# Kernel optimization log

Hardware: AMD Instinct MI355X
Metric: run time of the kernel (lower is better)

Reference implementation:

```python
import jax, jax.numpy as jnp
import numpy as np
from jax import lax

T, B, D, H = 1024, 64, 512, 1024


def setup_inputs() -> dict:
    key = jax.random.key(0)
    ks = jax.random.split(key, 5)
    x = jax.random.normal(ks[0], (T, B, D), dtype=jnp.float32)
    W_ih_0 = jax.random.normal(ks[1], (H, D), dtype=jnp.float32) * (1.0 / np.sqrt(D))
    w_hh_0 = jax.random.uniform(ks[2], (H,), dtype=jnp.float32)
    b_0 = jnp.zeros((H,), dtype=jnp.float32)
    W_ih_1 = jax.random.normal(ks[3], (H, H), dtype=jnp.float32) * (1.0 / np.sqrt(H))
    w_hh_1 = jax.random.uniform(ks[4], (H,), dtype=jnp.float32)
    b_1 = jnp.zeros((H,), dtype=jnp.float32)
    return {"x": x, "W_ih_0": W_ih_0, "w_hh_0": w_hh_0, "b_0": b_0,
            "W_ih_1": W_ih_1, "w_hh_1": w_hh_1, "b_1": b_1}


def _indrnn_layer(x, W_ih, w_hh, b):
    # Hoist the input projection into one batched GEMM over all timesteps.
    pre = jnp.einsum('tbd,hd->tbh', x, W_ih) + b  # [T,B,H]
    h0 = jnp.zeros((x.shape[1], W_ih.shape[0]), dtype=x.dtype)

    def step(h, p):
        h_new = jnp.tanh(p + h * w_hh)  # diagonal recurrence
        return h_new, h_new

    _, out = lax.scan(step, h0, pre)  # out: [T,B,H]
    return out


def reference(x, W_ih_0, w_hh_0, b_0, W_ih_1, w_hh_1, b_1):
    out0 = _indrnn_layer(x, W_ih_0, w_hh_0, b_0)
    out1 = _indrnn_layer(out0, W_ih_1, w_hh_1, b_1)
    # Original returns (last-layer outputs, initial hidden) -- hidden is
    # the unchanged zeros tensor of shape [num_layers, B, H].
    hidden = jnp.zeros((2, x.shape[1], W_ih_0.shape[0]), dtype=x.dtype)
    return out1, hidden
```

## Files before the change

### kernel.cpp

```cpp
#include <hip/hip_runtime.h>
#include <hip/hip_fp16.h>
#include <cstdint>
#include <cstddef>

#define TT 1024
#define BB 64
#define DD 512
#define HH 1024
#define MM (TT * BB)

typedef _Float16 f16;
typedef _Float16 f16x8 __attribute__((ext_vector_type(8)));
typedef float f32x4 __attribute__((ext_vector_type(4)));

__global__ void cvt_f32_to_f16(const float* __restrict__ src,
                               f16* __restrict__ dst, int n) {
    int i = blockIdx.x * blockDim.x + threadIdx.x;
    int idx = i * 8;
    if (idx + 8 <= n) {
        float4 a = *reinterpret_cast<const float4*>(src + idx);
        float4 b = *reinterpret_cast<const float4*>(src + idx + 4);
        f16x8 o;
        o[0] = (f16)a.x; o[1] = (f16)a.y; o[2] = (f16)a.z; o[3] = (f16)a.w;
        o[4] = (f16)b.x; o[5] = (f16)b.y; o[6] = (f16)b.z; o[7] = (f16)b.w;
        *reinterpret_cast<f16x8*>(dst + idx) = o;
    } else {
        for (int k = idx; k < n; ++k) dst[k] = (f16)src[k];
    }
}

__global__ void cvt_weights(const float* __restrict__ W0, f16* __restrict__ W0h,
                            int n0, const float* __restrict__ W1,
                            f16* __restrict__ W1h) {
    int i = blockIdx.x * blockDim.x + threadIdx.x;
    int idx = i * 8;
    const float* s;
    f16* d;
    int off;
    if (idx < n0) { s = W0; d = W0h; off = idx; }
    else          { s = W1; d = W1h; off = idx - n0; }
    float4 a = *reinterpret_cast<const float4*>(s + off);
    float4 b = *reinterpret_cast<const float4*>(s + off + 4);
    f16x8 o;
    o[0] = (f16)a.x; o[1] = (f16)a.y; o[2] = (f16)a.z; o[3] = (f16)a.w;
    o[4] = (f16)b.x; o[5] = (f16)b.y; o[6] = (f16)b.z; o[7] = (f16)b.w;
    *reinterpret_cast<f16x8*>(d + off) = o;
}

__device__ __forceinline__ void gload16(const void* g, void* l) {
    __builtin_amdgcn_global_load_lds(
        (const __attribute__((address_space(1))) void*)g,
        (__attribute__((address_space(3))) void*)l, 16, 0, 0);
}

__device__ __forceinline__ void stage128x64(const f16* __restrict__ G,
                                            int rowbase, int K, int kt,
                                            f16* lbuf, int tid) {
    #pragma unroll
    for (int j = 0; j < 4; ++j) {
        int p   = (j * 256 + tid) * 16;
        int row = p >> 7;
        int lc  = (p & 127) ^ ((row & 7) << 4);
        gload16(G + (size_t)(rowbase + row) * K + kt * 64 + (lc >> 1),
                (char*)lbuf + p);
    }
}

__device__ __forceinline__ f16x8 ldfrag(const f16* buf, int r, int s,
                                        int kg) {
    int c = ((s * 4 + kg) ^ (r & 7)) << 4;
    return *reinterpret_cast<const f16x8*>((const char*)buf + r * 128 + c);
}

template <typename TC>
__global__ __launch_bounds__(256, 4) void gemm5(
    const f16* __restrict__ A, const f16* __restrict__ W,
    const float* __restrict__ bias, TC* __restrict__ C,
    int M, int N, int K) {
    __shared__ f16 lds[2][128 * 64];

    const int tid  = threadIdx.x;
    const int lane = tid & 63;
    const int wid  = tid >> 6;
    const int wm   = wid >> 1;
    const int wn   = wid & 1;
    const int lr   = lane & 15;
    const int kg   = lane >> 4;

    const int nwg = gridDim.x;
    int bid = blockIdx.x;
    int wg  = (nwg % 8 == 0) ? ((bid & 7) * (nwg >> 3) + (bid >> 3)) : bid;
    const int ncol = N >> 7;
    const int brow = (wg / ncol) << 7;
    const int bcol = (wg % ncol) << 7;

    const int NT = K >> 6;

    f32x4 acc[4][4] = {};

    for (int t = 0; t < NT; ++t) {
        __syncthreads();
        stage128x64(A, brow, K, t, lds[0], tid);
        stage128x64(W, bcol, K, t, lds[1], tid);
        __syncthreads();

        #pragma unroll
        for (int s = 0; s < 2; ++s) {
            f16x8 af[4], bf[4];
            #pragma unroll
            for (int m = 0; m < 4; ++m)
                af[m] = ldfrag(lds[0], wm * 64 + m * 16 + lr, s, kg);
            #pragma unroll
            for (int n = 0; n < 4; ++n)
                bf[n] = ldfrag(lds[1], wn * 64 + n * 16 + lr, s, kg);
            #pragma unroll
            for (int m = 0; m < 4; ++m)
                #pragma unroll
                for (int n = 0; n < 4; ++n)
                    acc[m][n] = __builtin_amdgcn_mfma_f32_16x16x32_f16(
                        af[m], bf[n], acc[m][n], 0, 0, 0);
        }
    }

    if constexpr (sizeof(TC) == 2) {
        f16* Ct = &lds[0][0];
        __syncthreads();
        #pragma unroll
        for (int fn = 0; fn < 4; ++fn) {
            int col = wn * 64 + fn * 16 + lr;
            float bv = bias[bcol + col];
            #pragma unroll
            for (int fm = 0; fm < 4; ++fm) {
                int row0 = wm * 64 + fm * 16 + kg * 4;
                #pragma unroll
                for (int j = 0; j < 4; ++j) {
                    int r  = row0 + j;
                    int pb = r * 256 + ((col * 2) ^ ((r & 7) << 4));
                    *(f16*)((char*)Ct + pb) = (f16)(acc[fm][fn][j] + bv);
                }
            }
        }
        __syncthreads();
        #pragma unroll
        for (int i = 0; i < 8; ++i) {
            int e   = (i * 256 + tid) * 16;
            int row = e >> 8;
            int cb  = e & 255;
            int pb  = row * 256 + (cb ^ ((row & 7) << 4));
            f16x8 v = *(const f16x8*)((const char*)Ct + pb);
            *reinterpret_cast<f16x8*>(
                (f16*)C + (size_t)(brow + row) * N + bcol + (cb >> 1)) = v;
        }
    } else {
        #pragma unroll
        for (int fn = 0; fn < 4; ++fn) {
            int col = bcol + wn * 64 + fn * 16 + lr;
            float bv = bias[col];
            #pragma unroll
            for (int fm = 0; fm < 4; ++fm) {
                int row0 = brow + wm * 64 + fm * 16 + kg * 4;
                #pragma unroll
                for (int j = 0; j < 4; ++j)
                    C[(size_t)(row0 + j) * N + col] = (TC)(acc[fm][fn][j] + bv);
            }
        }
    }
}

__device__ __forceinline__ float fast_tanh(float x) {
    float e = __builtin_amdgcn_exp2f(x * 2.8853900817779268f);
    float r = __builtin_amdgcn_rcpf(e + 1.0f);
    return 1.0f - 2.0f * r;
}

template <typename TI, typename TO, int PF, bool ZTAIL>
__global__ __launch_bounds__(256) void scan_kernel(
    const TI* __restrict__ pre, const float* __restrict__ w,
    TO* __restrict__ out) {
    const int S = BB * HH;
    const int idx = blockIdx.x * blockDim.x + threadIdx.x;
    const float wv = w[idx & (HH - 1)];
    const TI* p = pre + idx;
    TO* o = out + idx;

    float buf[PF];
    #pragma unroll
    for (int i = 0; i < PF; ++i) buf[i] = (float)p[(size_t)i * S];

    float h = 0.f;
    for (int t0 = 0; t0 < TT; t0 += PF) {
        float nbuf[PF];
        #pragma unroll
        for (int i = 0; i < PF; ++i) {
            int tp = t0 + PF + i;
            tp = (tp < TT - 1) ? tp : (TT - 1);
            nbuf[i] = (float)p[(size_t)tp * S];
        }
        #pragma unroll
        for (int i = 0; i < PF; ++i) {
            h = fast_tanh(fmaf(h, wv, buf[i]));
            o[(size_t)(t0 + i) * S] = (TO)h;
        }
        #pragma unroll
        for (int i = 0; i < PF; ++i) buf[i] = nbuf[i];
    }
    if constexpr (ZTAIL) {
        o[(size_t)TT * S] = (TO)0.f;
        o[(size_t)(TT + 1) * S] = (TO)0.f;
    }
}

extern "C" void kernel_launch(void* const* d_in, const int* in_sizes, int n_in,
                              void* d_out, int out_size, void* d_ws, size_t ws_size,
                              hipStream_t stream) {
    const float* x  = (const float*)d_in[0];
    const float* W0 = (const float*)d_in[1];
    const float* w0 = (const float*)d_in[2];
    const float* b0 = (const float*)d_in[3];
    const float* W1 = (const float*)d_in[4];
    const float* w1 = (const float*)d_in[5];
    const float* b1 = (const float*)d_in[6];
    float* out = (float*)d_out;

    const size_t SZ_big = (size_t)MM * HH * sizeof(f16);
    const size_t O_W0   = SZ_big;
    const size_t O_W1   = O_W0 + (size_t)HH * DD * sizeof(f16);
    const size_t O_pre1 = O_W1 + (size_t)HH * HH * sizeof(f16);
    const bool f16pre1  = (ws_size >= O_pre1 + SZ_big);

    f16* big   = (f16*)d_ws;
    f16* W0h   = (f16*)((char*)d_ws + O_W0);
    f16* W1h   = (f16*)((char*)d_ws + O_W1);
    f16* pre1h = (f16*)((char*)d_ws + O_pre1);

    const int nwg = (MM / 128) * (HH / 128);

    cvt_f32_to_f16<<<(MM * DD) / 8 / 256, 256, 0, stream>>>(x, big, MM * DD);
    cvt_weights<<<(HH * DD + HH * HH) / 8 / 256, 256, 0, stream>>>(
        W0, W0h, HH * DD, W1, W1h);

    gemm5<f16><<<nwg, 256, 0, stream>>>(big, W0h, b0, (f16*)d_out, MM, HH, DD);

    scan_kernel<f16, f16, 32, false><<<(BB * HH) / 256, 256, 0, stream>>>(
        (const f16*)d_out, w0, big);

    if (f16pre1) {
        gemm5<f16><<<nwg, 256, 0, stream>>>(big, W1h, b1, pre1h, MM, HH, HH);
        scan_kernel<f16, float, 32, true><<<(BB * HH) / 256, 256, 0, stream>>>(
            pre1h, w1, out);
    } else {
        gemm5<float><<<nwg, 256, 0, stream>>>(big, W1h, b1, out, MM, HH, HH);
        scan_kernel<float, float, 32, true><<<(BB * HH) / 256, 256, 0, stream>>>(
            out, w1, out);
    }
}
```

Measured before the change: 425.4 us.

## Add 128x256-tile triple-buffered GEMM with split MFMA phases for layer-1 projection

Adds a new gemm8 kernel for the second layer's input projection (K=1024). It uses 512 threads, 128x256 output tiles and a three-stage LDS ring buffer, and staggers the A and B global-to-LDS loads between two MFMA half-phases. It also raises wave priority during the MFMA bursts. The aim is to increase per-tile data reuse and hide global load latency better than the 128x128 double-buffered gemm5. In exchange it uses 144KB of LDS, which allows only one workgroup per CU and halves the grid size. Only the f16 pre1 path uses it; the fp32 fallback still uses gemm5.

```diff
diff --git a/kernel.cpp b/kernel.cpp
--- a/kernel.cpp
+++ b/kernel.cpp
@@ -53,6 +53,12 @@
         (__attribute__((address_space(3))) void*)l, 16, 0, 0);
 }
 
+__device__ __forceinline__ f16x8 ldfrag(const f16* buf, int r, int s,
+                                        int kg) {
+    int c = ((s * 4 + kg) ^ (r & 7)) << 4;
+    return *reinterpret_cast<const f16x8*>((const char*)buf + r * 128 + c);
+}
+
 __device__ __forceinline__ void stage128x64(const f16* __restrict__ G,
                                             int rowbase, int K, int kt,
                                             f16* lbuf, int tid) {
@@ -64,12 +70,6 @@
         gload16(G + (size_t)(rowbase + row) * K + kt * 64 + (lc >> 1),
                 (char*)lbuf + p);
     }
-}
-
-__device__ __forceinline__ f16x8 ldfrag(const f16* buf, int r, int s,
-                                        int kg) {
-    int c = ((s * 4 + kg) ^ (r & 7)) << 4;
-    return *reinterpret_cast<const f16x8*>((const char*)buf + r * 128 + c);
 }
 
 template <typename TC>
@@ -164,6 +164,154 @@
                     C[(size_t)(row0 + j) * N + col] = (TC)(acc[fm][fn][j] + bv);
             }
         }
+    }
+}
+
+__device__ __forceinline__ void stageA8(const f16* __restrict__ G,
+                                        int rowbase, int K, int kt,
+                                        f16* lbuf, int tid) {
+    #pragma unroll
+    for (int j = 0; j < 2; ++j) {
+        int p   = (j * 512 + tid) * 16;
+        int row = p >> 7;
+        int lc  = (p & 127) ^ ((row & 7) << 4);
+        gload16(G + (size_t)(rowbase + row) * K + kt * 64 + (lc >> 1),
+                (char*)lbuf + p);
+    }
+}
+__device__ __forceinline__ void stageB8(const f16* __restrict__ G,
+                                        int rowbase, int K, int kt,
+                                        f16* lbuf, int tid) {
+    #pragma unroll
+    for (int j = 0; j < 4; ++j) {
+        int p   = (j * 512 + tid) * 16;
+        int row = p >> 7;
+        int lc  = (p & 127) ^ ((row & 7) << 4);
+        gload16(G + (size_t)(rowbase + row) * K + kt * 64 + (lc >> 1),
+                (char*)lbuf + p);
+    }
+}
+
+__global__ __launch_bounds__(512, 1) void gemm8(
+    const f16* __restrict__ A, const f16* __restrict__ W,
+    const float* __restrict__ bias, f16* __restrict__ C,
+    int M, int N, int K) {
+    __shared__ __align__(16) char smem[3 * 49152];
+
+    const int tid  = threadIdx.x;
+    const int lane = tid & 63;
+    const int wid  = tid >> 6;
+    const int wm   = wid >> 2;
+    const int wn   = wid & 3;
+    const int lr   = lane & 15;
+    const int kg   = lane >> 4;
+
+    const int nwg = gridDim.x;
+    int bid = blockIdx.x;
+    int wg  = (nwg % 8 == 0) ? ((bid & 7) * (nwg >> 3) + (bid >> 3)) : bid;
+    const int ncol = N >> 8;
+    const int brow = (wg / ncol) << 7;
+    const int bcol = (wg % ncol) << 8;
+
+    const int NT = K >> 6;
+
+    f32x4 acc[4][4] = {};
+
+    stageA8(A, brow, K, 0, (f16*)(smem +      0), tid);
+    stageB8(W, bcol, K, 0, (f16*)(smem +  16384), tid);
+    stageA8(A, brow, K, 1, (f16*)(smem +  49152), tid);
+    stageB8(W, bcol, K, 1, (f16*)(smem +  65536), tid);
+    asm volatile("s_waitcnt vmcnt(6)" ::: "memory");
+    __builtin_amdgcn_s_barrier();
+
+    for (int t = 0; t < NT; ++t) {
+        const int cs = t % 3;
+        const f16* As = (const f16*)(smem + cs * 49152);
+        const f16* Bs = (const f16*)(smem + cs * 49152 + 16384);
+        const int u  = t + 2;
+        const bool st = (u < NT);
+        const int us = u % 3;
+
+        f16x8 aA[4][2], bB[4][2];
+        #pragma unroll
+        for (int m = 0; m < 4; ++m)
+            #pragma unroll
+            for (int s = 0; s < 2; ++s)
+                aA[m][s] = ldfrag(As, wm * 64 + m * 16 + lr, s, kg);
+        #pragma unroll
+        for (int n = 0; n < 2; ++n)
+            #pragma unroll
+            for (int s = 0; s < 2; ++s)
+                bB[n][s] = ldfrag(Bs, wn * 64 + n * 16 + lr, s, kg);
+        if (st) stageA8(A, brow, K, u, (f16*)(smem + us * 49152), tid);
+        __builtin_amdgcn_s_barrier();
+        asm volatile("s_waitcnt lgkmcnt(0)" ::: "memory");
+        __builtin_amdgcn_sched_barrier(0);
+        __builtin_amdgcn_s_setprio(1);
+        #pragma unroll
+        for (int s = 0; s < 2; ++s)
+            #pragma unroll
+            for (int m = 0; m < 4; ++m)
+                #pragma unroll
+                for (int n = 0; n < 2; ++n)
+                    acc[m][n] = __builtin_amdgcn_mfma_f32_16x16x32_f16(
+                        aA[m][s], bB[n][s], acc[m][n], 0, 0, 0);
+        __builtin_amdgcn_s_setprio(0);
+        __builtin_amdgcn_sched_barrier(0);
+        __builtin_amdgcn_s_barrier();
+
+        #pragma unroll
+        for (int n = 0; n < 2; ++n)
+            #pragma unroll
+            for (int s = 0; s < 2; ++s)
+                bB[2 + n][s] = ldfrag(Bs, wn * 64 + (2 + n) * 16 + lr, s, kg);
+        if (st) stageB8(W, bcol, K, u, (f16*)(smem + us * 49152 + 16384), tid);
+        __builtin_amdgcn_s_barrier();
+        asm volatile("s_waitcnt lgkmcnt(0)" ::: "memory");
+        __builtin_amdgcn_sched_barrier(0);
+        __builtin_amdgcn_s_setprio(1);
+        #pragma unroll
+        for (int s = 0; s < 2; ++s)
+            #pragma unroll
+            for (int m = 0; m < 4; ++m)
+                #pragma unroll
+                for (int n = 0; n < 2; ++n)
+                    acc[m][2 + n] = __builtin_amdgcn_mfma_f32_16x16x32_f16(
+                        aA[m][s], bB[2 + n][s], acc[m][2 + n], 0, 0, 0);
+        __builtin_amdgcn_s_setprio(0);
+        __builtin_amdgcn_sched_barrier(0);
+        if (st)              { asm volatile("s_waitcnt vmcnt(6)" ::: "memory"); }
+        else if (t + 1 < NT) { asm volatile("s_waitcnt vmcnt(0)" ::: "memory"); }
+        __builtin_amdgcn_s_barrier();
+    }
+
+    f16* Ct = (f16*)smem;
+    __syncthreads();
+    #pragma unroll
+    for (int fn = 0; fn < 4; ++fn) {
+        int col = wn * 64 + fn * 16 + lr;
+        float bv = bias[bcol + col];
+        #pragma unroll
+        for (int fm = 0; fm < 4; ++fm) {
+            int row0 = wm * 64 + fm * 16 + kg * 4;
+            #pragma unroll
+            for (int j = 0; j < 4; ++j) {
+                int r  = row0 + j;
+                int pb = r * 512 + ((col * 2) ^ ((r & 7) << 4));
+                *(f16*)((char*)Ct + pb) = (f16)(acc[fm][fn][j] + bv);
+            }
+        }
+    }
+    __syncthreads();
+    #pragma unroll
+    for (int i = 0; i < 8; ++i) {
+        int e   = (i * 512 + tid) * 16;
+        int row = e >> 9;
+        int cb  = e & 511;
+        int pb  = row * 512 + (cb ^ ((row & 7) << 4));
+        f16x8 v = *(const f16x8*)((const char*)Ct + pb);
+        *reinterpret_cast<f16x8*>(
+            C + (size_t)(brow + row) * N + bcol + (cb >> 1)) = v;
     }
 }
 
@@ -233,23 +381,24 @@
     f16* W1h   = (f16*)((char*)d_ws + O_W1);
     f16* pre1h = (f16*)((char*)d_ws + O_pre1);
 
-    const int nwg = (MM / 128) * (HH / 128);
+    const int nwg5 = (MM / 128) * (HH / 128);
+    const int nwg8 = (MM / 128) * (HH / 256);
 
     cvt_f32_to_f16<<<(MM * DD) / 8 / 256, 256, 0, stream>>>(x, big, MM * DD);
     cvt_weights<<<(HH * DD + HH * HH) / 8 / 256, 256, 0, stream>>>(
         W0, W0h, HH * DD, W1, W1h);
 
-    gemm5<f16><<<nwg, 256, 0, stream>>>(big, W0h, b0, (f16*)d_out, MM, HH, DD);
+    gemm5<f16><<<nwg5, 256, 0, stream>>>(big, W0h, b0, (f16*)d_out, MM, HH, DD);
 
     scan_kernel<f16, f16, 32, false><<<(BB * HH) / 256, 256, 0, stream>>>(
         (const f16*)d_out, w0, big);
 
     if (f16pre1) {
-        gemm5<f16><<<nwg, 256, 0, stream>>>(big, W1h, b1, pre1h, MM, HH, HH);
+        gemm8<<<nwg8, 512, 0, stream>>>(big, W1h, b1, pre1h, MM, HH, HH);
         scan_kernel<f16, float, 32, true><<<(BB * HH) / 256, 256, 0, stream>>>(
             pre1h, w1, out);
     } else {
-        gemm5<float><<<nwg, 256, 0, stream>>>(big, W1h, b1, out, MM, HH, HH);
+        gemm5<float><<<nwg5, 256, 0, stream>>>(big, W1h, b1, out, MM, HH, HH);
         scan_kernel<float, float, 32, true><<<(BB * HH) / 256, 256, 0, stream>>>(
             out, w1, out);
     }
```

Result: slower. 456.3 us (+7.3%).
